# Kernel optimization log

Measured on AMD Instinct MI355X. Metric: run time of the kernel, lower is better.

The kernel has to match this reference:

```python
import jax, jax.numpy as jnp
import numpy as np

H = 1024  # hidden_size == batch (required by the original's (H,H) state init)
S = 128   # sequence length
I = 1024  # input_size


def setup_inputs() -> dict:
    key = jax.random.key(0)
    ks = jax.random.split(key, 9)
    def xavier(k, shape):
        fan_in, fan_out = shape
        limit = np.sqrt(6.0 / (fan_in + fan_out))
        return jax.random.uniform(k, shape, jnp.float32, -limit, limit)
    inp = {"x": jax.random.normal(ks[0], (H, S, I), jnp.float32)}
    names = ["w_ii", "w_hi", "w_if", "w_hf", "w_ig", "w_hg", "w_io", "w_ho"]
    dims = [(I, H), (H, H), (I, H), (H, H), (I, H), (H, H), (I, H), (H, H)]
    for n, d, k in zip(names, dims, ks[1:]):
        inp[n] = xavier(k, d)
    for n in ["b_ii", "b_hi", "b_if", "b_hf", "b_ig", "b_hg", "b_io", "b_ho"]:
        inp[n] = jnp.zeros((H,), jnp.float32)
    return inp


def reference(x, w_ii, b_ii, w_hi, b_hi, w_if, b_if, w_hf, b_hf,
              w_ig, b_ig, w_hg, b_hg, w_io, b_io, w_ho, b_ho):
    # Precompute input projections for all timesteps (same math, batched GEMM).
    # Shapes: (S, B, H) with B == H as in the original's broadcasting.
    xi = jnp.einsum('bsi,ih->sbh', x, w_ii) + b_ii + b_hi
    xf = jnp.einsum('bsi,ih->sbh', x, w_if) + b_if + b_hf
    xg = jnp.einsum('bsi,ih->sbh', x, w_ig) + b_ig + b_hg
    xo = jnp.einsum('bsi,ih->sbh', x, w_io) + b_io + b_ho

    h0 = jnp.zeros((w_hi.shape[0], w_hi.shape[1]), x.dtype)
    c0 = jnp.zeros_like(h0)

    def step(carry, xs):
        h, c = carry
        xi_t, xf_t, xg_t, xo_t = xs
        i = jax.nn.sigmoid(xi_t + h @ w_hi)
        f = jax.nn.sigmoid(xf_t + h @ w_hf)
        g = jnp.tanh(xg_t + h @ w_hg)
        o = jax.nn.sigmoid(xo_t + h @ w_ho)
        c = f * c + i * g
        h = o * jnp.tanh(c)
        return (h, c), None

    (h_t, c_t), _ = jax.lax.scan(step, (h0, c0), (xi, xf, xg, xo))
    return (h_t, c_t)
```

## Files before the change

kernel.cpp:

```cpp
#include <hip/hip_runtime.h>


#define Hdim 1024
#define Sdim 128
#define NBLK 256

typedef __attribute__((ext_vector_type(8))) short short8;
typedef __attribute__((ext_vector_type(4))) float floatx4;
typedef __attribute__((ext_vector_type(4))) unsigned short ushort4v;

#define GLDS(gp, lp)                                                     \
  __builtin_amdgcn_global_load_lds(                                      \
      (const __attribute__((address_space(1))) void*)(gp),               \
      (__attribute__((address_space(3))) void*)(lp), 16, 0, 0)

static __device__ __forceinline__ short f2bf(float f) {
  unsigned u = __float_as_uint(f);
  u += 0x7fffu + ((u >> 16) & 1u);
  return (short)(u >> 16);
}
static __device__ __forceinline__ float bf2f(unsigned short u) {
  return __uint_as_float((unsigned)u << 16);
}

__global__ __launch_bounds__(256) void wtrans(const float* __restrict__ src,
                                              unsigned short* __restrict__ dst) {
  __shared__ float tile[32][33];
  int h0 = blockIdx.x * 32, k0 = blockIdx.y * 32;
  int tx = threadIdx.x & 31, ty = threadIdx.x >> 5;
#pragma unroll
  for (int r = ty; r < 32; r += 8)
    tile[r][tx] = src[((size_t)(k0 + r) << 10) + h0 + tx];
  __syncthreads();
#pragma unroll
  for (int r = ty; r < 32; r += 8)
    dst[((size_t)(h0 + r) << 10) + k0 + tx] = (unsigned short)f2bf(tile[tx][r]);
}

__global__ void bias_combine(const float* __restrict__ b0, const float* __restrict__ b1,
                             const float* __restrict__ b2, const float* __restrict__ b3,
                             const float* __restrict__ b4, const float* __restrict__ b5,
                             const float* __restrict__ b6, const float* __restrict__ b7,
                             float* __restrict__ bias_c) {
  int i = blockIdx.x * 256 + threadIdx.x;
  int g = i >> 10, h = i & 1023;
  const float *pa, *pb;
  switch (g) {
    case 0: pa = b0; pb = b1; break;
    case 1: pa = b2; pb = b3; break;
    case 2: pa = b4; pb = b5; break;
    default: pa = b6; pb = b7; break;
  }
  bias_c[i] = pa[h] + pb[h];
}

__global__ __launch_bounds__(256) void xconv(const float* __restrict__ x,
                                             unsigned short* __restrict__ xb,
                                             int t0, int Tcur) {
  int tc = blockIdx.y;
  int tid8 = (blockIdx.x * 256 + threadIdx.x) * 8;
  int b = tid8 >> 10, k = tid8 & 1023;
  const float* src = x + ((((size_t)b << 7) + t0 + tc) << 10) + k;
  floatx4 f0 = *(const floatx4*)src;
  floatx4 f1 = *(const floatx4*)(src + 4);
  short8 o;
#pragma unroll
  for (int j = 0; j < 4; ++j) {
    o[j] = f2bf(f0[j]);
    o[4 + j] = f2bf(f1[j]);
  }
  *(short8*)(xb + (((size_t)b * Tcur + tc) << 10) + k) = o;
}

__global__ __launch_bounds__(256) void xgemm(const unsigned short* __restrict__ xb,
                                             const unsigned short* __restrict__ wT,
                                             unsigned short* __restrict__ xp,
                                             int Tcur) {
  __shared__ unsigned short As[128 * 32];
  __shared__ unsigned short Bs[128 * 32];
  int tid = threadIdx.x;
  int wave = tid >> 6, lane = tid & 63;
  int ln = lane & 15, lq = lane >> 4;
  int wm = wave & 1, wn = wave >> 1;
  int srow = lane >> 2, scol = (lane & 3) * 8;
  int nt = blockIdx.x;
  int g = nt >> 3;
  int h0 = (nt & 7) * 128;
  int mt = blockIdx.y;
  int tc = mt >> 3;
  int b0 = (mt & 7) * 128;
  const unsigned short* wx = wT + ((size_t)(2 * g) << 20);

  floatx4 acc[4][4];
#pragma unroll
  for (int i = 0; i < 4; ++i)
#pragma unroll
    for (int j = 0; j < 4; ++j) acc[i][j] = (floatx4){0.f, 0.f, 0.f, 0.f};

#pragma unroll 1
  for (int k0 = 0; k0 < 1024; k0 += 32) {
    __syncthreads();
#pragma unroll
    for (int i = 0; i < 2; ++i) {
      int q = wave * 2 + i;
      GLDS(xb + (((size_t)(b0 + q * 16 + srow) * Tcur + tc) << 10) + k0 + scol,
           (char*)As + q * 1024 + lane * 16);
      GLDS(wx + ((size_t)(h0 + q * 16 + srow) << 10) + k0 + scol,
           (char*)Bs + q * 1024 + lane * 16);
    }
    __syncthreads();
    short8 a[4], b[4];
#pragma unroll
    for (int i = 0; i < 4; ++i)
      a[i] = *(const short8*)(As + (wm * 64 + i * 16 + ln) * 32 + lq * 8);
#pragma unroll
    for (int j = 0; j < 4; ++j)
      b[j] = *(const short8*)(Bs + (wn * 64 + j * 16 + ln) * 32 + lq * 8);
#pragma unroll
    for (int i = 0; i < 4; ++i)
#pragma unroll
      for (int j = 0; j < 4; ++j)
        acc[i][j] = __builtin_amdgcn_mfma_f32_16x16x32_bf16(a[i], b[j], acc[i][j], 0, 0, 0);
  }

  size_t rowbase = (size_t)tc << 10;
#pragma unroll
  for (int i = 0; i < 4; ++i) {
    int brow = b0 + wm * 64 + i * 16 + lq * 4;
#pragma unroll
    for (int j = 0; j < 4; ++j) {
      int hcol = h0 + wn * 64 + j * 16 + ln;
#pragma unroll
      for (int r = 0; r < 4; ++r)
        xp[((rowbase + brow + r) << 12) + (hcol << 2) + g] =
            (unsigned short)f2bf(acc[i][j][r]);
    }
  }
}

__global__ __launch_bounds__(512, 2) void lstm_persist(
    const unsigned short* __restrict__ hA, unsigned short* __restrict__ hB,
    float* __restrict__ c_ws, const unsigned short* __restrict__ wT,
    const float* __restrict__ bias_c, const unsigned short* __restrict__ xp,
    float* __restrict__ out, unsigned* __restrict__ bar, unsigned bar_base,
    int t0, int Tcur, int save_c) {
  __shared__ unsigned short Wsh[4 * 16 * 1024];

  const int tid = threadIdx.x;
  const int bid = blockIdx.x;
  const int wave = tid >> 6, lane = tid & 63;
  const int ln = lane & 15, lq = lane >> 4;
  const int hc0 = (bid & 63) << 4;
  const int m0 = (bid >> 6) << 8;

  for (int c = tid; c < 8192; c += 512) {
    int g = c >> 11;
    int r = c & 2047;
    int hc = r >> 7;
    int kc = r & 127;
    short8 v = *(const short8*)(wT + (((size_t)(2 * g + 1)) << 20) +
                                ((size_t)(hc0 + hc) << 10) + kc * 8);
    unsigned byte = ((unsigned)(g * 16 + hc) << 11) + (unsigned)kc * 16;
    byte ^= (unsigned)(hc & 7) << 4;
    *(short8*)((char*)Wsh + byte) = v;
  }

  const int colh = hc0 + ln;
  const float bi = bias_c[colh];
  const float bff = bias_c[1024 + colh];
  const float bgc = bias_c[2048 + colh];
  const float bo = bias_c[3072 + colh];

  float creg[2][4];
#pragma unroll
  for (int i = 0; i < 2; ++i) {
    int row = m0 + wave * 32 + i * 16 + lq * 4;
#pragma unroll
    for (int r = 0; r < 4; ++r)
      creg[i][r] = c_ws[((size_t)(row + r) << 10) + colh];
  }

  __syncthreads();

  const unsigned short* hp = hA;
  unsigned short* hn = hB;

  floatx4 acc[4][2];
  const unsigned short *hrow0, *hrow1;

  auto loadch = [&](short8 (&buf)[2][2], int c) {
#pragma unroll
    for (int s = 0; s < 2; ++s) {
      buf[s][0] = *(const short8*)(hrow0 + c * 64 + s * 32);
      buf[s][1] = *(const short8*)(hrow1 + c * 64 + s * 32);
    }
  };
  auto compch = [&](short8 (&buf)[2][2], int c) {
#pragma unroll
    for (int s = 0; s < 2; ++s) {
      int kk = c * 64 + s * 32;
#pragma unroll
      for (int g = 0; g < 4; ++g) {
        unsigned byte = (((unsigned)(g * 16 + ln) << 11) + (unsigned)(kk + lq * 8) * 2) ^
                        ((unsigned)(ln & 7) << 4);
        short8 b = *(const short8*)((const char*)Wsh + byte);
#pragma unroll
        for (int i = 0; i < 2; ++i)
          acc[g][i] =
              __builtin_amdgcn_mfma_f32_16x16x32_bf16(buf[s][i], b, acc[g][i], 0, 0, 0);
      }
    }
  };

  for (int t = 0; t < Tcur; ++t) {
    ushort4v xpv[2][4];
#pragma unroll
    for (int i = 0; i < 2; ++i) {
      int rbase = m0 + wave * 32 + i * 16 + lq * 4;
#pragma unroll
      for (int r = 0; r < 4; ++r)
        xpv[i][r] = *(const ushort4v*)(xp + ((((size_t)t << 10) + rbase + r) << 12) +
                                       ((size_t)colh << 2));
    }

#pragma unroll
    for (int g = 0; g < 4; ++g)
#pragma unroll
      for (int i = 0; i < 2; ++i) acc[g][i] = (floatx4){0.f, 0.f, 0.f, 0.f};

    hrow0 = hp + ((size_t)(m0 + wave * 32 + ln) << 10) + lq * 8;
    hrow1 = hrow0 + (16 << 10);

    short8 aA[2][2], aB[2][2];
    loadch(aA, 0);
    loadch(aB, 1);
#pragma unroll 1
    for (int c = 0; c < 14; c += 2) {
      compch(aA, c);
      loadch(aA, c + 2);
      compch(aB, c + 1);
      loadch(aB, c + 3);
    }
    compch(aA, 14);
    compch(aB, 15);

    const int lastg = (t0 + t == Sdim - 1);
#pragma unroll
    for (int i = 0; i < 2; ++i) {
      int rbase2 = m0 + wave * 32 + i * 16 + lq * 4;
#pragma unroll
      for (int r = 0; r < 4; ++r) {
        int row = rbase2 + r;
        float pi = acc[0][i][r] + bf2f(xpv[i][r][0]) + bi;
        float pf = acc[1][i][r] + bf2f(xpv[i][r][1]) + bff;
        float pg = acc[2][i][r] + bf2f(xpv[i][r][2]) + bgc;
        float po = acc[3][i][r] + bf2f(xpv[i][r][3]) + bo;
        float gi = 1.f / (1.f + __expf(-pi));
        float gf = 1.f / (1.f + __expf(-pf));
        float gg = 2.f / (1.f + __expf(-2.f * pg)) - 1.f;
        float go = 1.f / (1.f + __expf(-po));
        float cn = gf * creg[i][r] + gi * gg;
        float hnv = go * (2.f / (1.f + __expf(-2.f * cn)) - 1.f);
        creg[i][r] = cn;
        size_t idx = ((size_t)row << 10) + colh;
        __hip_atomic_store(&hn[idx], (unsigned short)f2bf(hnv), __ATOMIC_RELAXED,
                           __HIP_MEMORY_SCOPE_AGENT);
        if (lastg) {
          out[idx] = hnv;
          out[(1u << 20) + idx] = cn;
        }
      }
    }

    if (t < Tcur - 1) {
      __syncthreads();
      if (tid == 0) {
        __hip_atomic_fetch_add(bar, 1u, __ATOMIC_RELAXED, __HIP_MEMORY_SCOPE_AGENT);
        unsigned tgt = bar_base + (unsigned)NBLK * (unsigned)(t + 1);
        while (__hip_atomic_load(bar, __ATOMIC_RELAXED, __HIP_MEMORY_SCOPE_AGENT) < tgt)
          __builtin_amdgcn_s_sleep(2);
        __builtin_amdgcn_fence(__ATOMIC_ACQUIRE, "agent");
      }
      __syncthreads();
    }

    unsigned short* tmp = hn;
    hn = (unsigned short*)hp;
    hp = tmp;
  }

  if (save_c) {
#pragma unroll
    for (int i = 0; i < 2; ++i) {
      int row = m0 + wave * 32 + i * 16 + lq * 4;
#pragma unroll
      for (int r = 0; r < 4; ++r)
        c_ws[((size_t)(row + r) << 10) + colh] = creg[i][r];
    }
  }
}

extern "C" void kernel_launch(void* const* d_in, const int* in_sizes, int n_in,
                              void* d_out, int out_size, void* d_ws, size_t ws_size,
                              hipStream_t stream) {
  const float* x = (const float*)d_in[0];
  char* ws = (char*)d_ws;
  unsigned short* wT = (unsigned short*)ws;
  float* bias_c = (float*)(ws + (16u << 20));
  unsigned* bar = (unsigned*)(ws + (16u << 20) + (32u << 10));
  unsigned short* hb0 = (unsigned short*)(ws + (17u << 20));
  unsigned short* hb1 = (unsigned short*)(ws + (19u << 20));
  float* c_ws = (float*)(ws + (21u << 20));
  unsigned short* xb = (unsigned short*)(ws + (25u << 20));

  size_t base = 25u << 20;
  size_t per_t = 10u << 20;
  int Tc = 1;
  if (ws_size > base + per_t) {
    size_t t = (ws_size - base) / per_t;
    Tc = t > 128 ? 128 : (int)t;
  }
  unsigned short* xp = xb + ((size_t)Tc << 20);

  for (int j = 0; j < 8; ++j)
    wtrans<<<dim3(32, 32), 256, 0, stream>>>((const float*)d_in[1 + j],
                                             wT + ((size_t)j << 20));
  bias_combine<<<16, 256, 0, stream>>>(
      (const float*)d_in[9], (const float*)d_in[10], (const float*)d_in[11],
      (const float*)d_in[12], (const float*)d_in[13], (const float*)d_in[14],
      (const float*)d_in[15], (const float*)d_in[16], bias_c);

  hipMemsetAsync(hb0, 0, 2u << 20, stream);
  hipMemsetAsync(c_ws, 0, 4u << 20, stream);
  hipMemsetAsync(bar, 0, 256, stream);

  float* out = (float*)d_out;
  unsigned short* hcur = hb0;
  unsigned short* hnxt = hb1;
  unsigned barcnt = 0;
  for (int t0 = 0; t0 < Sdim; t0 += Tc) {
    int Tcur = (Sdim - t0) < Tc ? (Sdim - t0) : Tc;
    xconv<<<dim3(512, Tcur), 256, 0, stream>>>(x, xb, t0, Tcur);
    xgemm<<<dim3(32, Tcur * 8), 256, 0, stream>>>(xb, wT, xp, Tcur);
    int save_c = (t0 + Tcur < Sdim) ? 1 : 0;
    lstm_persist<<<dim3(NBLK), dim3(512), 0, stream>>>(
        hcur, hnxt, c_ws, wT, bias_c, xp, out, bar,
        (unsigned)NBLK * barcnt, t0, Tcur, save_c);
    barcnt += (unsigned)(Tcur - 1);
    if (Tcur & 1) {
      unsigned short* tmp = hcur;
      hcur = hnxt;
      hnxt = tmp;
    }
  }
}
```

Baseline: 5.724 ms.

## Split global grid barrier into per-row-group barriers and deepen h prefetch

Replaces the single grid-wide barrier across all 256 blocks with four independent barriers, one per 256-row batch group of 64 blocks. This works because each row group's recurrence only depends on its own h rows. Block indices are remapped so each group's blocks are interleaved across the grid. The h-operand prefetch pipeline is deepened from two to four register buffers, which raises register pressure. The goal is to cut barrier contention and wait skew and to hide more load latency, at the cost of a larger barrier memset and more VGPRs.

```diff
diff --git a/kernel.cpp b/kernel.cpp
--- a/kernel.cpp
+++ b/kernel.cpp
@@ -150,18 +150,21 @@
   const int bid = blockIdx.x;
   const int wave = tid >> 6, lane = tid & 63;
   const int ln = lane & 15, lq = lane >> 4;
-  const int hc0 = (bid & 63) << 4;
-  const int m0 = (bid >> 6) << 8;
+  const int mg = (bid & 7) >> 1;
+  const int hc = ((bid >> 3) << 1) | (bid & 1);
+  const int hc0 = hc << 4;
+  const int m0 = mg << 8;
+  unsigned* gbar = bar + (mg << 6);
 
   for (int c = tid; c < 8192; c += 512) {
     int g = c >> 11;
     int r = c & 2047;
-    int hc = r >> 7;
+    int hcr = r >> 7;
     int kc = r & 127;
     short8 v = *(const short8*)(wT + (((size_t)(2 * g + 1)) << 20) +
-                                ((size_t)(hc0 + hc) << 10) + kc * 8);
-    unsigned byte = ((unsigned)(g * 16 + hc) << 11) + (unsigned)kc * 16;
-    byte ^= (unsigned)(hc & 7) << 4;
+                                ((size_t)(hc0 + hcr) << 10) + kc * 8);
+    unsigned byte = ((unsigned)(g * 16 + hcr) << 11) + (unsigned)kc * 16;
+    byte ^= (unsigned)(hcr & 7) << 4;
     *(short8*)((char*)Wsh + byte) = v;
   }
 
@@ -231,18 +234,26 @@
     hrow0 = hp + ((size_t)(m0 + wave * 32 + ln) << 10) + lq * 8;
     hrow1 = hrow0 + (16 << 10);
 
-    short8 aA[2][2], aB[2][2];
+    short8 aA[2][2], aB[2][2], aC[2][2], aD[2][2];
     loadch(aA, 0);
     loadch(aB, 1);
+    loadch(aC, 2);
+    loadch(aD, 3);
 #pragma unroll 1
-    for (int c = 0; c < 14; c += 2) {
+    for (int c = 0; c < 12; c += 4) {
       compch(aA, c);
-      loadch(aA, c + 2);
+      loadch(aA, c + 4);
       compch(aB, c + 1);
-      loadch(aB, c + 3);
-    }
-    compch(aA, 14);
-    compch(aB, 15);
+      loadch(aB, c + 5);
+      compch(aC, c + 2);
+      loadch(aC, c + 6);
+      compch(aD, c + 3);
+      loadch(aD, c + 7);
+    }
+    compch(aA, 12);
+    compch(aB, 13);
+    compch(aC, 14);
+    compch(aD, 15);
 
     const int lastg = (t0 + t == Sdim - 1);
 #pragma unroll
@@ -275,9 +286,9 @@
     if (t < Tcur - 1) {
       __syncthreads();
       if (tid == 0) {
-        __hip_atomic_fetch_add(bar, 1u, __ATOMIC_RELAXED, __HIP_MEMORY_SCOPE_AGENT);
-        unsigned tgt = bar_base + (unsigned)NBLK * (unsigned)(t + 1);
-        while (__hip_atomic_load(bar, __ATOMIC_RELAXED, __HIP_MEMORY_SCOPE_AGENT) < tgt)
+        __hip_atomic_fetch_add(gbar, 1u, __ATOMIC_RELAXED, __HIP_MEMORY_SCOPE_AGENT);
+        unsigned tgt = (bar_base + (unsigned)(t + 1)) << 6;
+        while (__hip_atomic_load(gbar, __ATOMIC_RELAXED, __HIP_MEMORY_SCOPE_AGENT) < tgt)
           __builtin_amdgcn_s_sleep(2);
         __builtin_amdgcn_fence(__ATOMIC_ACQUIRE, "agent");
       }
@@ -332,7 +343,7 @@
 
   hipMemsetAsync(hb0, 0, 2u << 20, stream);
   hipMemsetAsync(c_ws, 0, 4u << 20, stream);
-  hipMemsetAsync(bar, 0, 256, stream);
+  hipMemsetAsync(bar, 0, 4096, stream);
 
   float* out = (float*)d_out;
   unsigned short* hcur = hb0;
@@ -344,8 +355,7 @@
     xgemm<<<dim3(32, Tcur * 8), 256, 0, stream>>>(xb, wT, xp, Tcur);
     int save_c = (t0 + Tcur < Sdim) ? 1 : 0;
     lstm_persist<<<dim3(NBLK), dim3(512), 0, stream>>>(
-        hcur, hnxt, c_ws, wT, bias_c, xp, out, bar,
-        (unsigned)NBLK * barcnt, t0, Tcur, save_c);
+        hcur, hnxt, c_ws, wT, bias_c, xp, out, bar, barcnt, t0, Tcur, save_c);
     barcnt += (unsigned)(Tcur - 1);
     if (Tcur & 1) {
       unsigned short* tmp = hcur;
```

Result: faster. 5.299 ms (-7.4%).
